# Performance work log

Hardware: AMD Instinct MI355X
Metric: run time of the kernel (lower is better)

The kernel has to match this reference:

```python
import jax, jax.numpy as jnp
import numpy as np

B, BITS, HID = 4096, 64, 512
EPS = 1e-5
TEMPERATURE = 1.0  # buffer default


def _w(k, shape):
    return jax.random.normal(k, shape, jnp.float32) * 0.02


def setup_inputs() -> dict:
    key = jax.random.key(0)
    ks = jax.random.split(key, 8)
    return {
        "a_bits": jax.random.uniform(ks[0], (B, BITS), jnp.float32),
        "shift_bits": jax.random.uniform(ks[1], (B, BITS), jnp.float32),
        # shift_decoder params
        "W1": _w(ks[2], (HID, BITS)), "b1": jnp.zeros((HID,), jnp.float32),
        "g1": jnp.ones((HID,), jnp.float32), "be1": jnp.zeros((HID,), jnp.float32),
        "W2": _w(ks[3], (HID, HID)), "b2": jnp.zeros((HID,), jnp.float32),
        "g2": jnp.ones((HID,), jnp.float32), "be2": jnp.zeros((HID,), jnp.float32),
        "W3": _w(ks[4], (BITS, HID)), "b3": jnp.zeros((BITS,), jnp.float32),
        # index_net params (input dim = 2*BITS)
        "Wi1": _w(ks[5], (HID, 2 * BITS)), "bi1": jnp.zeros((HID,), jnp.float32),
        "Wi2": _w(ks[6], (HID, HID)), "bi2": jnp.zeros((HID,), jnp.float32),
        "Wi3": _w(ks[7], (BITS, HID)), "bi3": jnp.zeros((BITS,), jnp.float32),
    }


def _layernorm(x, g, b):
    m = jnp.mean(x, axis=-1, keepdims=True)
    v = jnp.mean(jnp.square(x - m), axis=-1, keepdims=True)
    return (x - m) * jax.lax.rsqrt(v + EPS) * g + b


def reference(a_bits, shift_bits, W1, b1, g1, be1, W2, b2, g2, be2, W3, b3,
              Wi1, bi1, Wi2, bi2, Wi3, bi3):
    # shift decoder: Linear -> LN -> ReLU -> Linear -> LN -> ReLU -> Linear
    h = jax.nn.relu(_layernorm(shift_bits @ W1.T + b1, g1, be1))
    h = jax.nn.relu(_layernorm(h @ W2.T + b2, g2, be2))
    shift_logits = h @ W3.T + b3                        # [B, BITS]
    shift_soft = jax.nn.softmax(shift_logits / TEMPERATURE, axis=-1)

    # index_net, vectorized over the output-position loop.
    # combined = [one_hot(i), shift_soft]; the one-hot part of the first Linear
    # just selects column i of Wi1[:, :BITS], so we add it as a [BITS, HID] bias.
    pos_part = Wi1[:, :BITS].T                          # [BITS, HID]
    shift_part = shift_soft @ Wi1[:, BITS:].T           # [B, HID]
    h1 = jax.nn.relu(pos_part[None, :, :] + shift_part[:, None, :] + bi1)  # [B, BITS, HID]
    h2 = jax.nn.relu(jnp.einsum('bph,kh->bpk', h1, Wi2) + bi2)             # [B, BITS, HID]
    idx_logits = jnp.einsum('bph,kh->bpk', h2, Wi3) + bi3                  # [B, BITS, BITS]
    idx_soft = jax.nn.softmax(idx_logits / TEMPERATURE, axis=-1)

    # softmax-weighted gather-sum over a_bits
    return jnp.einsum('bpj,bj->bp', idx_soft, a_bits)   # [B, BITS]
```

## Files before the change

kernel.cpp:

```cpp
#include <hip/hip_runtime.h>
#include <hip/hip_bf16.h>
#include <math.h>

#define B_N 4096
#define BITSN 64
#define HID 512
#define EPSV 1e-5f
#define BT 16

typedef unsigned short ushort_t;
typedef __attribute__((ext_vector_type(8))) short bf16x8;
typedef __attribute__((ext_vector_type(4))) float f32x4;
typedef __attribute__((ext_vector_type(16))) float f32x16;

__device__ __forceinline__ ushort_t f2bf(float f) {
  unsigned u = __float_as_uint(f);
  u += 0x7FFF + ((u >> 16) & 1);
  return (ushort_t)(u >> 16);
}

__device__ __forceinline__ unsigned pack2bf(float lo, float hi) {
  union { __hip_bfloat162 h; unsigned u; } cv;
  cv.h = __float22bfloat162_rn(make_float2(lo, hi));
  return cv.u;
}

__global__ __launch_bounds__(256) void prep_kernel(
    const float* __restrict__ Wi2, const float* __restrict__ Wi3,
    const float* __restrict__ Wi1, const float* __restrict__ W1,
    const float* __restrict__ W2, const float* __restrict__ W3,
    float* __restrict__ Wi1posT, ushort_t* __restrict__ W1b,
    ushort_t* __restrict__ W2b, ushort_t* __restrict__ W3b,
    ushort_t* __restrict__ Wi1sb, ushort_t* __restrict__ Wi2f32,
    ushort_t* __restrict__ Wi3f) {
  int idx = blockIdx.x * 256 + threadIdx.x;
  if (idx < 512 * 512) {
    W2b[idx] = f2bf(W2[idx]);
    int j = idx & 7, lane = (idx >> 3) & 63;
    int ct = (idx >> 9) & 15, ks = idx >> 13;
    int c = ct * 32 + (lane & 31);
    int k = ks * 16 + (lane >> 5) * 8 + j;
    Wi2f32[idx] = f2bf(Wi2[c * 512 + k]);
  }
  if (idx < 64 * 512) {
    W3b[idx] = f2bf(W3[idx]);
    int p = idx >> 9, i = idx & 511;
    Wi1posT[idx] = Wi1[i * 128 + p];
    int j = idx & 7, lane = (idx >> 3) & 63;
    int nt = (idx >> 9) & 3, ks2 = idx >> 11;
    int jr = nt * 16 + (lane & 15);
    int k = ks2 * 32 + (lane >> 4) * 8 + j;
    Wi3f[idx] = f2bf(Wi3[jr * 512 + k]);
  }
  if (idx < 512 * 64) {
    W1b[idx] = f2bf(W1[idx]);
    int j = idx >> 6, k = idx & 63;
    Wi1sb[idx] = f2bf(Wi1[j * 128 + 64 + k]);
  }
}

__global__ __launch_bounds__(256) void shift2_kernel(
    const float* __restrict__ shift_bits,
    const ushort_t* __restrict__ W1b, const float* __restrict__ b1,
    const float* __restrict__ g1, const float* __restrict__ be1,
    const ushort_t* __restrict__ W2b, const float* __restrict__ b2,
    const float* __restrict__ g2, const float* __restrict__ be2,
    const ushort_t* __restrict__ W3b, const float* __restrict__ b3,
    const ushort_t* __restrict__ Wi1sb, const float* __restrict__ bi1,
    float* __restrict__ sp) {
  __shared__ __align__(16) ushort_t hA[BT * 512];
  __shared__ __align__(16) char reg2[32 * 1024];
  __shared__ float b1s[512], g1s[512], be1s[512];
  __shared__ float b2s[512], g2s[512], be2s[512], bi1s[512];
  __shared__ float red[4][BT][2];
  __shared__ float b3s[64];

  ushort_t* sbt = (ushort_t*)reg2;
  ushort_t* Bs  = (ushort_t*)reg2;
  ushort_t* h2  = (ushort_t*)reg2;
  float (*lg32)[68] = (float(*)[68])(reg2 + 16 * 1024);
  ushort_t* sb2 = (ushort_t*)(reg2 + 16 * 1024 + 16 * 68 * 4);

  int b0 = blockIdx.x * BT;
  int t = threadIdx.x, w = t >> 6, l = t & 63, lg = l >> 4, l15 = l & 15;

  b1s[t] = b1[t];  b1s[t + 256] = b1[t + 256];
  g1s[t] = g1[t];  g1s[t + 256] = g1[t + 256];
  be1s[t] = be1[t]; be1s[t + 256] = be1[t + 256];
  b2s[t] = b2[t];  b2s[t + 256] = b2[t + 256];
  g2s[t] = g2[t];  g2s[t + 256] = g2[t + 256];
  be2s[t] = be2[t]; be2s[t + 256] = be2[t + 256];
  bi1s[t] = bi1[t]; bi1s[t + 256] = bi1[t + 256];
  if (t < 64) b3s[t] = b3[t];
  if (t < 128) {
    int row = t >> 3, g = t & 7;
    const float* src = shift_bits + (size_t)(b0 + row) * 64 + g * 8;
    uint4 pk;
    pk.x = (unsigned)f2bf(src[0]) | ((unsigned)f2bf(src[1]) << 16);
    pk.y = (unsigned)f2bf(src[2]) | ((unsigned)f2bf(src[3]) << 16);
    pk.z = (unsigned)f2bf(src[4]) | ((unsigned)f2bf(src[5]) << 16);
    pk.w = (unsigned)f2bf(src[6]) | ((unsigned)f2bf(src[7]) << 16);
    *(uint4*)((char*)sbt + ((row * 128 + g * 16) ^ ((row & 7) << 4))) = pk;
  }
  __syncthreads();

  f32x4 acc[8];
#pragma unroll
  for (int nt = 0; nt < 8; ++nt) acc[nt] = (f32x4){0.f, 0.f, 0.f, 0.f};
#pragma unroll
  for (int ks = 0; ks < 2; ++ks) {
    bf16x8 af = *(const bf16x8*)((char*)sbt + ((l15 * 128 + ks * 64 + lg * 16) ^ ((l15 & 7) << 4)));
#pragma unroll
    for (int nt = 0; nt < 8; ++nt) {
      int c = w * 128 + nt * 16 + l15;
      bf16x8 bfr = *(const bf16x8*)(W1b + (size_t)c * 64 + ks * 32 + lg * 8);
      acc[nt] = __builtin_amdgcn_mfma_f32_16x16x32_bf16(af, bfr, acc[nt], 0, 0, 0);
    }
  }
  {
    float s[4] = {0.f, 0.f, 0.f, 0.f}, q[4] = {0.f, 0.f, 0.f, 0.f};
#pragma unroll
    for (int nt = 0; nt < 8; ++nt) {
      int c = w * 128 + nt * 16 + l15;
      float bb = b1s[c];
#pragma unroll
      for (int r = 0; r < 4; ++r) {
        float x = acc[nt][r] + bb;
        acc[nt][r] = x;
        s[r] += x; q[r] += x * x;
      }
    }
#pragma unroll
    for (int m = 8; m >= 1; m >>= 1)
#pragma unroll
      for (int r = 0; r < 4; ++r) { s[r] += __shfl_xor(s[r], m); q[r] += __shfl_xor(q[r], m); }
    if (l15 == 0)
#pragma unroll
      for (int r = 0; r < 4; ++r) { red[w][4 * lg + r][0] = s[r]; red[w][4 * lg + r][1] = q[r]; }
    __syncthreads();
    float mean[4], rs[4];
#pragma unroll
    for (int r = 0; r < 4; ++r) {
      int p = 4 * lg + r;
      float S = red[0][p][0] + red[1][p][0] + red[2][p][0] + red[3][p][0];
      float Q = red[0][p][1] + red[1][p][1] + red[2][p][1] + red[3][p][1];
      mean[r] = S * (1.0f / 512.0f);
      float var = Q * (1.0f / 512.0f) - mean[r] * mean[r];
      rs[r] = rsqrtf(var + EPSV);
    }
#pragma unroll
    for (int nt = 0; nt < 8; ++nt) {
      int c = w * 128 + nt * 16 + l15;
      float gg = g1s[c], bb = be1s[c];
#pragma unroll
      for (int r = 0; r < 4; ++r) {
        int p = 4 * lg + r;
        float v = (acc[nt][r] - mean[r]) * rs[r] * gg + bb;
        v = v > 0.f ? v : 0.f;
        *(ushort_t*)((char*)hA + ((p * 1024 + c * 2) ^ ((p & 7) << 4))) = f2bf(v);
      }
    }
  }
  __syncthreads();

#pragma unroll
  for (int nt = 0; nt < 8; ++nt) acc[nt] = (f32x4){0.f, 0.f, 0.f, 0.f};
  for (int step = 0; step < 16; ++step) {
    int i0 = step * 32;
#pragma unroll
    for (int qq = 0; qq < 8; ++qq) {
      int g = qq * 256 + t;
      int c = g >> 2, xg = g & 3;
      int ic = xg ^ ((c >> 1) & 3);
      ((uint4*)Bs)[g] = *(const uint4*)(W2b + (size_t)c * 512 + i0 + ic * 8);
    }
    __syncthreads();
    bf16x8 af = *(const bf16x8*)((char*)hA + ((l15 * 1024 + step * 64 + lg * 16) ^ ((l15 & 7) << 4)));
#pragma unroll
    for (int nt = 0; nt < 8; ++nt) {
      int c = w * 128 + nt * 16 + l15;
      bf16x8 bfr = ((const bf16x8*)Bs)[c * 4 + (lg ^ ((c >> 1) & 3))];
      acc[nt] = __builtin_amdgcn_mfma_f32_16x16x32_bf16(af, bfr, acc[nt], 0, 0, 0);
    }
    __syncthreads();
  }
  {
    float s[4] = {0.f, 0.f, 0.f, 0.f}, q[4] = {0.f, 0.f, 0.f, 0.f};
#pragma unroll
    for (int nt = 0; nt < 8; ++nt) {
      int c = w * 128 + nt * 16 + l15;
      float bb = b2s[c];
#pragma unroll
      for (int r = 0; r < 4; ++r) {
        float x = acc[nt][r] + bb;
        acc[nt][r] = x;
        s[r] += x; q[r] += x * x;
      }
    }
#pragma unroll
    for (int m = 8; m >= 1; m >>= 1)
#pragma unroll
      for (int r = 0; r < 4; ++r) { s[r] += __shfl_xor(s[r], m); q[r] += __shfl_xor(q[r], m); }
    if (l15 == 0)
#pragma unroll
      for (int r = 0; r < 4; ++r) { red[w][4 * lg + r][0] = s[r]; red[w][4 * lg + r][1] = q[r]; }
    __syncthreads();
    float mean[4], rs[4];
#pragma unroll
    for (int r = 0; r < 4; ++r) {
      int p = 4 * lg + r;
      float S = red[0][p][0] + red[1][p][0] + red[2][p][0] + red[3][p][0];
      float Q = red[0][p][1] + red[1][p][1] + red[2][p][1] + red[3][p][1];
      mean[r] = S * (1.0f / 512.0f);
      float var = Q * (1.0f / 512.0f) - mean[r] * mean[r];
      rs[r] = rsqrtf(var + EPSV);
    }
#pragma unroll
    for (int nt = 0; nt < 8; ++nt) {
      int c = w * 128 + nt * 16 + l15;
      float gg = g2s[c], bb = be2s[c];
#pragma unroll
      for (int r = 0; r < 4; ++r) {
        int p = 4 * lg + r;
        float v = (acc[nt][r] - mean[r]) * rs[r] * gg + bb;
        v = v > 0.f ? v : 0.f;
        *(ushort_t*)((char*)h2 + ((p * 1024 + c * 2) ^ ((p & 7) << 4))) = f2bf(v);
      }
    }
  }
  __syncthreads();

  {
    f32x4 a3 = (f32x4){0.f, 0.f, 0.f, 0.f};
#pragma unroll
    for (int ks = 0; ks < 16; ++ks) {
      bf16x8 af = *(const bf16x8*)((char*)h2 + ((l15 * 1024 + ks * 64 + lg * 16) ^ ((l15 & 7) << 4)));
      bf16x8 bfr = *(const bf16x8*)(W3b + (size_t)(w * 16 + l15) * 512 + ks * 32 + lg * 8);
      a3 = __builtin_amdgcn_mfma_f32_16x16x32_bf16(af, bfr, a3, 0, 0, 0);
    }
    int c = w * 16 + l15;
    float bb = b3s[c];
#pragma unroll
    for (int r = 0; r < 4; ++r) lg32[4 * lg + r][c] = a3[r] + bb;
  }
  __syncthreads();

  {
    int r = t >> 4, j = t & 15;
    float v[4];
    float m = -1e30f;
#pragma unroll
    for (int mq = 0; mq < 4; ++mq) { v[mq] = lg32[r][mq * 16 + j]; m = fmaxf(m, v[mq]); }
#pragma unroll
    for (int mk = 8; mk >= 1; mk >>= 1) m = fmaxf(m, __shfl_xor(m, mk));
    float ssum = 0.f;
#pragma unroll
    for (int mq = 0; mq < 4; ++mq) { v[mq] = expf(v[mq] - m); ssum += v[mq]; }
#pragma unroll
    for (int mk = 8; mk >= 1; mk >>= 1) ssum += __shfl_xor(ssum, mk);
    float inv = 1.f / ssum;
#pragma unroll
    for (int mq = 0; mq < 4; ++mq) {
      int c = mq * 16 + j;
      *(ushort_t*)((char*)sb2 + ((r * 128 + c * 2) ^ ((r & 7) << 4))) = f2bf(v[mq] * inv);
    }
  }
  __syncthreads();

  {
    f32x4 a4[8];
#pragma unroll
    for (int nt = 0; nt < 8; ++nt) a4[nt] = (f32x4){0.f, 0.f, 0.f, 0.f};
#pragma unroll
    for (int ks = 0; ks < 2; ++ks) {
      bf16x8 af = *(const bf16x8*)((char*)sb2 + ((l15 * 128 + ks * 64 + lg * 16) ^ ((l15 & 7) << 4)));
#pragma unroll
      for (int nt = 0; nt < 8; ++nt) {
        int c = w * 128 + nt * 16 + l15;
        bf16x8 bfr = *(const bf16x8*)(Wi1sb + (size_t)c * 64 + ks * 32 + lg * 8);
        a4[nt] = __builtin_amdgcn_mfma_f32_16x16x32_bf16(af, bfr, a4[nt], 0, 0, 0);
      }
    }
#pragma unroll
    for (int nt = 0; nt < 8; ++nt) {
      int c = w * 128 + nt * 16 + l15;
      float bb = bi1s[c];
#pragma unroll
      for (int r = 0; r < 4; ++r)
        sp[(size_t)(b0 + 4 * lg + r) * 512 + c] = a4[nt][r] + bb;
    }
  }
}

__global__ __launch_bounds__(512, 4) void big6_kernel(
    const float* __restrict__ a_bits, const float* __restrict__ sp,
    const float* __restrict__ Wi1posT,
    const ushort_t* __restrict__ Wi2f32, const ushort_t* __restrict__ Wi3f,
    const float* __restrict__ bi2, const float* __restrict__ bi3,
    float* __restrict__ out) {
  __shared__ __align__(16) ushort_t h1s[64 * 512];
  __shared__ float bi2s[512];
  __shared__ float ab[64];
  __shared__ float bi3s[64];

  int b = blockIdx.x, t = threadIdx.x;
  int w = t >> 6, l = t & 63, lg = l >> 4, l15 = l & 15;
  int l31 = l & 31, hi = l >> 5;

  bi2s[t] = bi2[t];
  if (t < 64) { ab[t] = a_bits[b * 64 + t]; bi3s[t] = bi3[t]; }

  {
    const float* sprow = sp + (size_t)b * 512 + l * 8;
    float4 s0 = *(const float4*)(sprow);
    float4 s1 = *(const float4*)(sprow + 4);
#pragma unroll
    for (int g = 0; g < 8; ++g) {
      int p = g * 8 + w;
      const float4* pr = (const float4*)(Wi1posT + (size_t)p * 512 + l * 8);
      float4 p0 = pr[0], p1 = pr[1];
      float v0 = fmaxf(s0.x + p0.x, 0.f), v1 = fmaxf(s0.y + p0.y, 0.f);
      float v2 = fmaxf(s0.z + p0.z, 0.f), v3 = fmaxf(s0.w + p0.w, 0.f);
      float v4 = fmaxf(s1.x + p1.x, 0.f), v5 = fmaxf(s1.y + p1.y, 0.f);
      float v6 = fmaxf(s1.z + p1.z, 0.f), v7 = fmaxf(s1.w + p1.w, 0.f);
      uint4 pk;
      pk.x = pack2bf(v0, v1); pk.y = pack2bf(v2, v3);
      pk.z = pack2bf(v4, v5); pk.w = pack2bf(v6, v7);
      *(uint4*)((char*)h1s + ((p * 1024 + l * 16) ^ ((p & 15) << 4))) = pk;
    }
  }
  __syncthreads();

  f32x16 acc[2][2];
#pragma unroll
  for (int mc = 0; mc < 2; ++mc)
#pragma unroll
    for (int np = 0; np < 2; ++np)
#pragma unroll
      for (int r = 0; r < 16; ++r) acc[mc][np][r] = 0.f;

  const bf16x8* bbase = (const bf16x8*)Wi2f32 + ((size_t)(2 * w) * 64 + l);
  bf16x8 wf[4][2];
#pragma unroll
  for (int d = 0; d < 4; ++d) {
    wf[d][0] = bbase[(size_t)d * 1024];
    wf[d][1] = bbase[(size_t)d * 1024 + 64];
  }

  for (int kb = 0; kb < 8; ++kb) {
#pragma unroll
    for (int d = 0; d < 4; ++d) {
      int ks = kb * 4 + d;
      bf16x8 w0 = wf[d][0], w1 = wf[d][1];
      if (kb < 7) {
        wf[d][0] = bbase[(size_t)(ks + 4) * 1024];
        wf[d][1] = bbase[(size_t)(ks + 4) * 1024 + 64];
      }
      int row0 = l31, row1 = 32 + l31;
      bf16x8 h0 = *(const bf16x8*)((char*)h1s + ((row0 * 1024 + ks * 32 + hi * 16) ^ ((row0 & 15) << 4)));
      bf16x8 h1v = *(const bf16x8*)((char*)h1s + ((row1 * 1024 + ks * 32 + hi * 16) ^ ((row1 & 15) << 4)));
      acc[0][0] = __builtin_amdgcn_mfma_f32_32x32x16_bf16(w0, h0, acc[0][0], 0, 0, 0);
      acc[0][1] = __builtin_amdgcn_mfma_f32_32x32x16_bf16(w0, h1v, acc[0][1], 0, 0, 0);
      acc[1][0] = __builtin_amdgcn_mfma_f32_32x32x16_bf16(w1, h0, acc[1][0], 0, 0, 0);
      acc[1][1] = __builtin_amdgcn_mfma_f32_32x32x16_bf16(w1, h1v, acc[1][1], 0, 0, 0);
    }
  }
  __syncthreads();

#pragma unroll
  for (int mc = 0; mc < 2; ++mc) {
#pragma unroll
    for (int np = 0; np < 2; ++np) {
      int p = np * 32 + l31;
#pragma unroll
      for (int rq = 0; rq < 4; ++rq) {
        int c0 = w * 64 + mc * 32 + 8 * rq + 4 * hi;
        float4 bi4 = *(const float4*)(bi2s + c0);
        float v0 = fmaxf(acc[mc][np][4 * rq + 0] + bi4.x, 0.f);
        float v1 = fmaxf(acc[mc][np][4 * rq + 1] + bi4.y, 0.f);
        float v2 = fmaxf(acc[mc][np][4 * rq + 2] + bi4.z, 0.f);
        float v3 = fmaxf(acc[mc][np][4 * rq + 3] + bi4.w, 0.f);
        uint2 pk;
        pk.x = pack2bf(v0, v1);
        pk.y = pack2bf(v2, v3);
        *(uint2*)((char*)h1s + ((p * 1024 + c0 * 2) ^ ((p & 15) << 4))) = pk;
      }
    }
  }
  __syncthreads();

  if (w < 4) {
    f32x4 lacc[4];
#pragma unroll
    for (int n = 0; n < 4; ++n) lacc[n] = (f32x4){0.f, 0.f, 0.f, 0.f};
    int p2 = 16 * w + l15;
    const bf16x8* b3base = (const bf16x8*)Wi3f + l;
#pragma unroll 4
    for (int ks2 = 0; ks2 < 16; ++ks2) {
      bf16x8 a2 = *(const bf16x8*)((char*)h1s + ((p2 * 1024 + ks2 * 64 + lg * 16) ^ ((p2 & 15) << 4)));
#pragma unroll
      for (int nt2 = 0; nt2 < 4; ++nt2) {
        bf16x8 b2v = b3base[(ks2 * 4 + nt2) * 64];
        lacc[nt2] = __builtin_amdgcn_mfma_f32_16x16x32_bf16(a2, b2v, lacc[nt2], 0, 0, 0);
      }
    }

#pragma unroll
    for (int r = 0; r < 4; ++r) {
      float v[4];
      float m = -1e30f;
#pragma unroll
      for (int nt2 = 0; nt2 < 4; ++nt2) {
        v[nt2] = lacc[nt2][r] + bi3s[nt2 * 16 + l15];
        m = fmaxf(m, v[nt2]);
      }
#pragma unroll
      for (int mm = 8; mm >= 1; mm >>= 1) m = fmaxf(m, __shfl_xor(m, mm));
      float s = 0.f, g = 0.f;
#pragma unroll
      for (int nt2 = 0; nt2 < 4; ++nt2) {
        float e = expf(v[nt2] - m);
        s += e;
        g += e * ab[nt2 * 16 + l15];
      }
#pragma unroll
      for (int mm = 8; mm >= 1; mm >>= 1) { s += __shfl_xor(s, mm); g += __shfl_xor(g, mm); }
      if (l15 == 0) out[b * 64 + 16 * w + 4 * lg + r] = g / s;
    }
  }
}

extern "C" void kernel_launch(void* const* d_in, const int* in_sizes, int n_in,
                              void* d_out, int out_size, void* d_ws, size_t ws_size,
                              hipStream_t stream) {
  const float* a_bits     = (const float*)d_in[0];
  const float* shift_bits = (const float*)d_in[1];
  const float* W1  = (const float*)d_in[2];
  const float* b1  = (const float*)d_in[3];
  const float* g1  = (const float*)d_in[4];
  const float* be1 = (const float*)d_in[5];
  const float* W2  = (const float*)d_in[6];
  const float* b2  = (const float*)d_in[7];
  const float* g2  = (const float*)d_in[8];
  const float* be2 = (const float*)d_in[9];
  const float* W3  = (const float*)d_in[10];
  const float* b3  = (const float*)d_in[11];
  const float* Wi1 = (const float*)d_in[12];
  const float* bi1 = (const float*)d_in[13];
  const float* Wi2 = (const float*)d_in[14];
  const float* bi2 = (const float*)d_in[15];
  const float* Wi3 = (const float*)d_in[16];
  const float* bi3 = (const float*)d_in[17];
  float* out = (float*)d_out;

  float* sp = (float*)d_ws;
  ushort_t* W2b = (ushort_t*)((char*)d_ws + (size_t)B_N * HID * 4);
  ushort_t* W1b = W2b + 512 * 512;
  ushort_t* W3b = W1b + 512 * 64;
  ushort_t* Wi1sb = W3b + 64 * 512;
  float* Wi1posT = (float*)(Wi1sb + 512 * 64);
  ushort_t* Wi2f32 = (ushort_t*)(Wi1posT + 64 * 512);
  ushort_t* Wi3f = Wi2f32 + 512 * 512;

  prep_kernel<<<1024, 256, 0, stream>>>(Wi2, Wi3, Wi1, W1, W2, W3,
                                        Wi1posT, W1b, W2b, W3b, Wi1sb, Wi2f32, Wi3f);
  shift2_kernel<<<B_N / BT, 256, 0, stream>>>(shift_bits, W1b, b1, g1, be1,
                                              W2b, b2, g2, be2, W3b, b3, Wi1sb, bi1, sp);
  big6_kernel<<<B_N, 512, 0, stream>>>(a_bits, sp, Wi1posT, Wi2f32, Wi3f, bi2, bi3, out);
}
```

Baseline: 213.1 us.

## Feed second-layer accumulators straight into the third MFMA via register fragments

The h2 accumulators stay in registers and are packed as bf16 A-operand fragments for the Wi3 GEMM, instead of being written to LDS and reread by half the waves. Wi3 is pre-permuted to match this fragment layout, so all 8 waves do the third GEMM over their own K-slice. Partial logits are combined with LDS float atomics, and the softmax drops the max subtraction and uses the fast exp. This also adds s_setprio around the MFMA groups. It removes an LDS round trip and idle waves, but adds atomic contention and risks overflow in the unshifted exp.

```diff
diff --git a/kernel.cpp b/kernel.cpp
--- a/kernel.cpp
+++ b/kernel.cpp
@@ -32,7 +32,7 @@
     float* __restrict__ Wi1posT, ushort_t* __restrict__ W1b,
     ushort_t* __restrict__ W2b, ushort_t* __restrict__ W3b,
     ushort_t* __restrict__ Wi1sb, ushort_t* __restrict__ Wi2f32,
-    ushort_t* __restrict__ Wi3f) {
+    ushort_t* __restrict__ Wi3g) {
   int idx = blockIdx.x * 256 + threadIdx.x;
   if (idx < 512 * 512) {
     W2b[idx] = f2bf(W2[idx]);
@@ -46,11 +46,12 @@
     W3b[idx] = f2bf(W3[idx]);
     int p = idx >> 9, i = idx & 511;
     Wi1posT[idx] = Wi1[i * 128 + p];
-    int j = idx & 7, lane = (idx >> 3) & 63;
-    int nt = (idx >> 9) & 3, ks2 = idx >> 11;
-    int jr = nt * 16 + (lane & 15);
-    int k = ks2 * 32 + (lane >> 4) * 8 + j;
-    Wi3f[idx] = f2bf(Wi3[jr * 512 + k]);
+    int e = idx & 7, lane = (idx >> 3) & 63;
+    int jt = (idx >> 9) & 1, h = (idx >> 10) & 1;
+    int mc = (idx >> 11) & 1, w = idx >> 12;
+    int jr = jt * 32 + (lane & 31);
+    int c = w * 64 + mc * 32 + 16 * h + 4 * (lane >> 5) + (e & 3) + 8 * (e >> 2);
+    Wi3g[idx] = f2bf(Wi3[jr * 512 + c]);
   }
   if (idx < 512 * 64) {
     W1b[idx] = f2bf(W1[idx]);
@@ -292,10 +293,10 @@
   }
 }
 
-__global__ __launch_bounds__(512, 4) void big6_kernel(
+__global__ __launch_bounds__(512, 4) void big7_kernel(
     const float* __restrict__ a_bits, const float* __restrict__ sp,
     const float* __restrict__ Wi1posT,
-    const ushort_t* __restrict__ Wi2f32, const ushort_t* __restrict__ Wi3f,
+    const ushort_t* __restrict__ Wi2f32, const ushort_t* __restrict__ Wi3g,
     const float* __restrict__ bi2, const float* __restrict__ bi3,
     float* __restrict__ out) {
   __shared__ __align__(16) ushort_t h1s[64 * 512];
@@ -304,7 +305,7 @@
   __shared__ float bi3s[64];
 
   int b = blockIdx.x, t = threadIdx.x;
-  int w = t >> 6, l = t & 63, lg = l >> 4, l15 = l & 15;
+  int w = t >> 6, l = t & 63;
   int l31 = l & 31, hi = l >> 5;
 
   bi2s[t] = bi2[t];
@@ -339,94 +340,119 @@
 #pragma unroll
       for (int r = 0; r < 16; ++r) acc[mc][np][r] = 0.f;
 
-  const bf16x8* bbase = (const bf16x8*)Wi2f32 + ((size_t)(2 * w) * 64 + l);
-  bf16x8 wf[4][2];
-#pragma unroll
-  for (int d = 0; d < 4; ++d) {
-    wf[d][0] = bbase[(size_t)d * 1024];
-    wf[d][1] = bbase[(size_t)d * 1024 + 64];
-  }
-
-  for (int kb = 0; kb < 8; ++kb) {
+  {
+    const bf16x8* bbase = (const bf16x8*)Wi2f32 + ((size_t)(2 * w) * 64 + l);
+    bf16x8 wf[4][2];
 #pragma unroll
     for (int d = 0; d < 4; ++d) {
-      int ks = kb * 4 + d;
-      bf16x8 w0 = wf[d][0], w1 = wf[d][1];
-      if (kb < 7) {
-        wf[d][0] = bbase[(size_t)(ks + 4) * 1024];
-        wf[d][1] = bbase[(size_t)(ks + 4) * 1024 + 64];
-      }
-      int row0 = l31, row1 = 32 + l31;
-      bf16x8 h0 = *(const bf16x8*)((char*)h1s + ((row0 * 1024 + ks * 32 + hi * 16) ^ ((row0 & 15) << 4)));
-      bf16x8 h1v = *(const bf16x8*)((char*)h1s + ((row1 * 1024 + ks * 32 + hi * 16) ^ ((row1 & 15) << 4)));
-      acc[0][0] = __builtin_amdgcn_mfma_f32_32x32x16_bf16(w0, h0, acc[0][0], 0, 0, 0);
-      acc[0][1] = __builtin_amdgcn_mfma_f32_32x32x16_bf16(w0, h1v, acc[0][1], 0, 0, 0);
-      acc[1][0] = __builtin_amdgcn_mfma_f32_32x32x16_bf16(w1, h0, acc[1][0], 0, 0, 0);
-      acc[1][1] = __builtin_amdgcn_mfma_f32_32x32x16_bf16(w1, h1v, acc[1][1], 0, 0, 0);
-    }
-  }
-  __syncthreads();
-
+      wf[d][0] = bbase[(size_t)d * 1024];
+      wf[d][1] = bbase[(size_t)d * 1024 + 64];
+    }
+    for (int kb = 0; kb < 8; ++kb) {
+#pragma unroll
+      for (int d = 0; d < 4; ++d) {
+        int ks = kb * 4 + d;
+        bf16x8 w0 = wf[d][0], w1 = wf[d][1];
+        if (kb < 7) {
+          wf[d][0] = bbase[(size_t)(ks + 4) * 1024];
+          wf[d][1] = bbase[(size_t)(ks + 4) * 1024 + 64];
+        }
+        int row0 = l31, row1 = 32 + l31;
+        bf16x8 h0 = *(const bf16x8*)((char*)h1s + ((row0 * 1024 + ks * 32 + hi * 16) ^ ((row0 & 15) << 4)));
+        bf16x8 h1v = *(const bf16x8*)((char*)h1s + ((row1 * 1024 + ks * 32 + hi * 16) ^ ((row1 & 15) << 4)));
+        __builtin_amdgcn_s_setprio(1);
+        acc[0][0] = __builtin_amdgcn_mfma_f32_32x32x16_bf16(w0, h0, acc[0][0], 0, 0, 0);
+        acc[0][1] = __builtin_amdgcn_mfma_f32_32x32x16_bf16(w0, h1v, acc[0][1], 0, 0, 0);
+        acc[1][0] = __builtin_amdgcn_mfma_f32_32x32x16_bf16(w1, h0, acc[1][0], 0, 0, 0);
+        acc[1][1] = __builtin_amdgcn_mfma_f32_32x32x16_bf16(w1, h1v, acc[1][1], 0, 0, 0);
+        __builtin_amdgcn_s_setprio(0);
+      }
+    }
+  }
+
+  bf16x8 pkf[2][2][2];
 #pragma unroll
   for (int mc = 0; mc < 2; ++mc) {
+    float bia[16];
+#pragma unroll
+    for (int rq = 0; rq < 4; ++rq) {
+      int c0 = w * 64 + mc * 32 + 8 * rq + 4 * hi;
+      float4 bi4 = *(const float4*)(bi2s + c0);
+      bia[4 * rq + 0] = bi4.x; bia[4 * rq + 1] = bi4.y;
+      bia[4 * rq + 2] = bi4.z; bia[4 * rq + 3] = bi4.w;
+    }
 #pragma unroll
     for (int np = 0; np < 2; ++np) {
-      int p = np * 32 + l31;
-#pragma unroll
-      for (int rq = 0; rq < 4; ++rq) {
-        int c0 = w * 64 + mc * 32 + 8 * rq + 4 * hi;
-        float4 bi4 = *(const float4*)(bi2s + c0);
-        float v0 = fmaxf(acc[mc][np][4 * rq + 0] + bi4.x, 0.f);
-        float v1 = fmaxf(acc[mc][np][4 * rq + 1] + bi4.y, 0.f);
-        float v2 = fmaxf(acc[mc][np][4 * rq + 2] + bi4.z, 0.f);
-        float v3 = fmaxf(acc[mc][np][4 * rq + 3] + bi4.w, 0.f);
-        uint2 pk;
-        pk.x = pack2bf(v0, v1);
-        pk.y = pack2bf(v2, v3);
-        *(uint2*)((char*)h1s + ((p * 1024 + c0 * 2) ^ ((p & 15) << 4))) = pk;
-      }
-    }
-  }
-  __syncthreads();
-
-  if (w < 4) {
-    f32x4 lacc[4];
-#pragma unroll
-    for (int n = 0; n < 4; ++n) lacc[n] = (f32x4){0.f, 0.f, 0.f, 0.f};
-    int p2 = 16 * w + l15;
-    const bf16x8* b3base = (const bf16x8*)Wi3f + l;
-#pragma unroll 4
-    for (int ks2 = 0; ks2 < 16; ++ks2) {
-      bf16x8 a2 = *(const bf16x8*)((char*)h1s + ((p2 * 1024 + ks2 * 64 + lg * 16) ^ ((p2 & 15) << 4)));
-#pragma unroll
-      for (int nt2 = 0; nt2 < 4; ++nt2) {
-        bf16x8 b2v = b3base[(ks2 * 4 + nt2) * 64];
-        lacc[nt2] = __builtin_amdgcn_mfma_f32_16x16x32_bf16(a2, b2v, lacc[nt2], 0, 0, 0);
-      }
-    }
-
-#pragma unroll
-    for (int r = 0; r < 4; ++r) {
-      float v[4];
-      float m = -1e30f;
-#pragma unroll
-      for (int nt2 = 0; nt2 < 4; ++nt2) {
-        v[nt2] = lacc[nt2][r] + bi3s[nt2 * 16 + l15];
-        m = fmaxf(m, v[nt2]);
-      }
-#pragma unroll
-      for (int mm = 8; mm >= 1; mm >>= 1) m = fmaxf(m, __shfl_xor(m, mm));
-      float s = 0.f, g = 0.f;
-#pragma unroll
-      for (int nt2 = 0; nt2 < 4; ++nt2) {
-        float e = expf(v[nt2] - m);
-        s += e;
-        g += e * ab[nt2 * 16 + l15];
-      }
-#pragma unroll
-      for (int mm = 8; mm >= 1; mm >>= 1) { s += __shfl_xor(s, mm); g += __shfl_xor(g, mm); }
-      if (l15 == 0) out[b * 64 + 16 * w + 4 * lg + r] = g / s;
-    }
+      float hv[16];
+#pragma unroll
+      for (int r = 0; r < 16; ++r) hv[r] = fmaxf(acc[mc][np][r] + bia[r], 0.f);
+#pragma unroll
+      for (int h = 0; h < 2; ++h) {
+        unsigned d0 = pack2bf(hv[8 * h + 0], hv[8 * h + 1]);
+        unsigned d1 = pack2bf(hv[8 * h + 2], hv[8 * h + 3]);
+        unsigned d2 = pack2bf(hv[8 * h + 4], hv[8 * h + 5]);
+        unsigned d3 = pack2bf(hv[8 * h + 6], hv[8 * h + 7]);
+        union { unsigned u[4]; bf16x8 v; } cv;
+        cv.u[0] = d0; cv.u[1] = d1; cv.u[2] = d2; cv.u[3] = d3;
+        pkf[np][mc][h] = cv.v;
+      }
+    }
+  }
+  __syncthreads();
+
+  float* Lg = (float*)h1s;
+  {
+    int p = t >> 3, jo = t & 7;
+    float4 bA = *(const float4*)(bi3s + jo * 8);
+    float4 bB = *(const float4*)(bi3s + jo * 8 + 4);
+    *(float4*)(Lg + p * 64 + jo * 8) = bA;
+    *(float4*)(Lg + p * 64 + jo * 8 + 4) = bB;
+  }
+  __syncthreads();
+
+  {
+    const bf16x8* gbase = (const bf16x8*)Wi3g + ((size_t)w * 8 * 64 + l);
+    f32x16 l00, l01, l10, l11;
+#pragma unroll
+    for (int r = 0; r < 16; ++r) { l00[r] = 0.f; l01[r] = 0.f; l10[r] = 0.f; l11[r] = 0.f; }
+#pragma unroll
+    for (int mc = 0; mc < 2; ++mc) {
+#pragma unroll
+      for (int h = 0; h < 2; ++h) {
+        bf16x8 g0 = gbase[((mc * 2 + h) * 2 + 0) * 64];
+        bf16x8 g1 = gbase[((mc * 2 + h) * 2 + 1) * 64];
+        __builtin_amdgcn_s_setprio(1);
+        l00 = __builtin_amdgcn_mfma_f32_32x32x16_bf16(pkf[0][mc][h], g0, l00, 0, 0, 0);
+        l01 = __builtin_amdgcn_mfma_f32_32x32x16_bf16(pkf[0][mc][h], g1, l01, 0, 0, 0);
+        l10 = __builtin_amdgcn_mfma_f32_32x32x16_bf16(pkf[1][mc][h], g0, l10, 0, 0, 0);
+        l11 = __builtin_amdgcn_mfma_f32_32x32x16_bf16(pkf[1][mc][h], g1, l11, 0, 0, 0);
+        __builtin_amdgcn_s_setprio(0);
+      }
+    }
+#pragma unroll
+    for (int r = 0; r < 16; ++r) {
+      int prow = (r & 3) + 8 * (r >> 2) + 4 * hi;
+      atomicAdd(Lg + (prow)      * 64 + l31,      l00[r]);
+      atomicAdd(Lg + (prow)      * 64 + 32 + l31, l01[r]);
+      atomicAdd(Lg + (prow + 32) * 64 + l31,      l10[r]);
+      atomicAdd(Lg + (prow + 32) * 64 + 32 + l31, l11[r]);
+    }
+  }
+  __syncthreads();
+
+  {
+    int p = t >> 3, jo = t & 7;
+    float4 vA = *(const float4*)(Lg + p * 64 + jo * 8);
+    float4 vB = *(const float4*)(Lg + p * 64 + jo * 8 + 4);
+    const float* abp = ab + jo * 8;
+    float e0 = __expf(vA.x), e1 = __expf(vA.y), e2 = __expf(vA.z), e3 = __expf(vA.w);
+    float e4 = __expf(vB.x), e5 = __expf(vB.y), e6 = __expf(vB.z), e7 = __expf(vB.w);
+    float s = e0 + e1 + e2 + e3 + e4 + e5 + e6 + e7;
+    float g = e0 * abp[0] + e1 * abp[1] + e2 * abp[2] + e3 * abp[3]
+            + e4 * abp[4] + e5 * abp[5] + e6 * abp[6] + e7 * abp[7];
+#pragma unroll
+    for (int mm = 4; mm >= 1; mm >>= 1) { s += __shfl_xor(s, mm); g += __shfl_xor(g, mm); }
+    if (jo == 0) out[b * 64 + p] = g / s;
   }
 }
 
@@ -460,11 +486,11 @@
   ushort_t* Wi1sb = W3b + 64 * 512;
   float* Wi1posT = (float*)(Wi1sb + 512 * 64);
   ushort_t* Wi2f32 = (ushort_t*)(Wi1posT + 64 * 512);
-  ushort_t* Wi3f = Wi2f32 + 512 * 512;
+  ushort_t* Wi3g = Wi2f32 + 512 * 512;
 
   prep_kernel<<<1024, 256, 0, stream>>>(Wi2, Wi3, Wi1, W1, W2, W3,
-                                        Wi1posT, W1b, W2b, W3b, Wi1sb, Wi2f32, Wi3f);
+                                        Wi1posT, W1b, W2b, W3b, Wi1sb, Wi2f32, Wi3g);
   shift2_kernel<<<B_N / BT, 256, 0, stream>>>(shift_bits, W1b, b1, g1, be1,
                                               W2b, b2, g2, be2, W3b, b3, Wi1sb, bi1, sp);
-  big6_kernel<<<B_N, 512, 0, stream>>>(a_bits, sp, Wi1posT, Wi2f32, Wi3f, bi2, bi3, out);
-}
+  big7_kernel<<<B_N, 512, 0, stream>>>(a_bits, sp, Wi1posT, Wi2f32, Wi3g, bi2, bi3, out);
+}
```

Result: slower. 818.7 us (+284.1%).
